# Kernel tuning notes

Measured on AMD Instinct MI355X. Metric: run time of the kernel, lower is better.

## Reference

```python
import jax, jax.numpy as jnp
import numpy as np

B, LAT, ADIM, NACT, H = 131072, 64, 16, 9, 128

def setup_inputs() -> dict:
    key = jax.random.key(0)
    ks = jax.random.split(key, 24)
    p = lambda k, shp: (jax.random.normal(k, shp, dtype=jnp.float32) * 0.05)
    return {
        "z_t": jax.random.normal(ks[0], (B, LAT), dtype=jnp.float32),
        "action": jax.random.randint(ks[1], (B,), 0, NACT),
        "hidden": jnp.zeros((1, B, H), dtype=jnp.float32),
        "embed": p(ks[2], (NACT, ADIM)),
        "fuse_W": p(ks[3], (H, LAT + ADIM)), "fuse_b": p(ks[4], (H,)),
        "W_ih": p(ks[5], (3 * H, H)), "W_hh": p(ks[6], (3 * H, H)),
        "b_ih": p(ks[7], (3 * H,)), "b_hh": p(ks[8], (3 * H,)),
        "ns_W1": p(ks[9], (H, H)), "ns_b1": p(ks[10], (H,)),
        "ns_W2": p(ks[11], (LAT, H)), "ns_b2": p(ks[12], (LAT,)),
        "rw_W1": p(ks[13], (H // 2, H)), "rw_b1": p(ks[14], (H // 2,)),
        "rw_W2": p(ks[15], (1, H // 2)), "rw_b2": p(ks[16], (1,)),
        "dn_W1": p(ks[17], (H // 2, H)), "dn_b1": p(ks[18], (H // 2,)),
        "dn_W2": p(ks[19], (1, H // 2)), "dn_b2": p(ks[20], (1,)),
    }

def _mlp2(x, W1, b1, W2, b2):
    return jax.nn.relu(x @ W1.T + b1) @ W2.T + b2

def reference(z_t, action, hidden, embed, fuse_W, fuse_b, W_ih, W_hh, b_ih, b_hh,
              ns_W1, ns_b1, ns_W2, ns_b2, rw_W1, rw_b1, rw_W2, rw_b2,
              dn_W1, dn_b1, dn_W2, dn_b2):
    a_emb = embed[action]                                  # [B, ADIM]
    fused = jnp.concatenate([z_t, a_emb], axis=-1)         # [B, LAT+ADIM]
    x = jax.nn.relu(fused @ fuse_W.T + fuse_b)             # [B, H]
    h0 = hidden[0]                                         # [B, H]
    gi = x @ W_ih.T + b_ih                                 # [B, 3H]
    gh = h0 @ W_hh.T + b_hh                                # [B, 3H]
    Hd = x.shape[-1]
    r = jax.nn.sigmoid(gi[:, :Hd] + gh[:, :Hd])
    zg = jax.nn.sigmoid(gi[:, Hd:2 * Hd] + gh[:, Hd:2 * Hd])
    n = jnp.tanh(gi[:, 2 * Hd:] + r * gh[:, 2 * Hd:])
    h_new = (1.0 - zg) * n + zg * h0                       # [B, H]
    out = h_new
    z_next = _mlp2(out, ns_W1, ns_b1, ns_W2, ns_b2)        # [B, LAT]
    reward = _mlp2(out, rw_W1, rw_b1, rw_W2, rw_b2)        # [B, 1]
    done_logit = _mlp2(out, dn_W1, dn_b1, dn_W2, dn_b2)    # [B, 1]
    return (z_next, reward, done_logit, h_new[None])
```

## Files before the change

kernel.cpp:

```cpp
#include <hip/hip_runtime.h>
#include <hip/hip_bf16.h>
#include <cstddef>
#include <cstdint>

#define BATCH 131072
#define HOFF ((size_t)BATCH * 66)

typedef __attribute__((ext_vector_type(8))) short short8;
typedef __attribute__((ext_vector_type(4))) short short4v;
typedef __attribute__((ext_vector_type(4))) float f32x4;

typedef const __attribute__((address_space(1))) unsigned int* gas_t;
typedef __attribute__((address_space(3))) unsigned int* las_t;

#define WS_GRU   13312
#define WS_HEAD  119808
#define WS_ELEMS 165888

#define MFMA(a,b,c) __builtin_amdgcn_mfma_f32_16x16x32_bf16((a),(b),(c),0,0,0)

__device__ __forceinline__ short f2bf(float x) {
    __hip_bfloat16 b = __float2bfloat16(x);
    return __builtin_bit_cast(short, b);
}
__device__ __forceinline__ float bf2f(short s) {
    unsigned u = ((unsigned)(unsigned short)s) << 16;
    return __builtin_bit_cast(float, u);
}
__device__ __forceinline__ float fsigmoid(float x) { return __builtin_amdgcn_rcpf(1.0f + __expf(-x)); }
__device__ __forceinline__ float ftanh(float x)    { return 1.0f - 2.0f * __builtin_amdgcn_rcpf(1.0f + __expf(2.0f * x)); }

__device__ __forceinline__ short8 packbf(f32x4 a, f32x4 b) {
    short8 r;
    r[0]=f2bf(a[0]); r[1]=f2bf(a[1]); r[2]=f2bf(a[2]); r[3]=f2bf(a[3]);
    r[4]=f2bf(b[0]); r[5]=f2bf(b[1]); r[6]=f2bf(b[2]); r[7]=f2bf(b[3]);
    return r;
}

template<int NCH>
__device__ __forceinline__ void stage_lds(const short* __restrict__ src, short* dst, int t) {
    constexpr int NP = (NCH + 511) / 512;
    #pragma unroll
    for (int k = 0; k < NP; ++k) {
        int c = t + 512 * k;
        if ((NCH % 512 == 0) || c < NCH)
            __builtin_amdgcn_global_load_lds((gas_t)(const void*)(src + (size_t)c * 8),
                                             (las_t)(void*)(dst + (size_t)c * 8), 16, 0, 0);
    }
}

extern "C" __global__ void prep_weights(const float* __restrict__ fuse_W,
                                        const float* __restrict__ W_ih, const float* __restrict__ W_hh,
                                        const float* __restrict__ ns_W1, const float* __restrict__ ns_W2,
                                        const float* __restrict__ rw_W1, const float* __restrict__ dn_W1,
                                        short* __restrict__ ws) {
    int i = blockIdx.x * 256 + threadIdx.x;
    if (i >= WS_ELEMS) return;
    float v = 0.f;
    if (i < WS_GRU) {
        int j = i / 104, k = i % 104;
        if (k < 80) v = fuse_W[j*80 + k];
    } else if (i < WS_HEAD) {
        int g = (i - WS_GRU) / 6656, e = (i - WS_GRU) % 6656;
        int r = e / 136, k = e % 136;
        if (r < 48 && k < 128) {
            int j = g >> 1;
            const float* W = (g & 1) ? W_hh : W_ih;
            int gate = r >> 4, rr = r & 15;
            v = W[(size_t)(gate*128 + j*16 + rr)*128 + k];
        }
    } else {
        int h = (i - WS_HEAD) / 4608, e = (i - WS_HEAD) % 4608;
        int r = e / 136, k = e % 136;
        if (r < 32 && k < 128) {
            const float* W; int rb;
            if (h < 4)      { W = ns_W1; rb = h*32; }
            else if (h < 6) { W = ns_W2; rb = (h-4)*32; }
            else if (h < 8) { W = rw_W1; rb = (h-6)*32; }
            else            { W = dn_W1; rb = (h-8)*32; }
            v = W[(size_t)(rb + r)*128 + k];
        }
    }
    ws[i] = f2bf(v);
}

#define HEAD_GEMM(FRAG, BIAS, Q, HALFOFF, SP, RELU) do {                                   \
    _Pragma("unroll") for (int sub = 0; sub < 2; ++sub) {                                  \
        float bb = (BIAS)[(Q)*32 + sub*16 + lo];                                           \
        f32x4 a0 = zz4, a1 = zz4;                                                          \
        _Pragma("unroll") for (int kt = 0; kt < 4; ++kt) {                                 \
            short8 Bf = *(const short8*)&smem[(HALFOFF) + (sub*16+lo)*136 + kt*32 + hi*8]; \
            a0 = MFMA((FRAG)[0][kt], Bf, a0); a1 = MFMA((FRAG)[1][kt], Bf, a1); }          \
        _Pragma("unroll") for (int e = 0; e < 4; ++e) {                                    \
            float v0 = a0[e] + bb, v1 = a1[e] + bb;                                        \
            if (RELU) { v0 = fmaxf(v0, 0.f); v1 = fmaxf(v1, 0.f); }                        \
            (SP)[(4*hi+e)*40 + sub*16 + lo]      = f2bf(v0);                               \
            (SP)[(16+4*hi+e)*40 + sub*16 + lo]   = f2bf(v1); }                             \
    } } while (0)

#define AFRAG_READ(DST, Q, SP) do {                                    \
    (DST)[0][Q] = *(const short8*)&(SP)[lo*40 + hi*8];                 \
    (DST)[1][Q] = *(const short8*)&(SP)[(16+lo)*40 + hi*8]; } while (0)

extern "C" __global__ __launch_bounds__(512, 2)
void gru_mfma(const float* __restrict__ z_t, const int* __restrict__ action,
              const float* __restrict__ hidden, const float* __restrict__ embed,
              const float* __restrict__ fuse_b,
              const float* __restrict__ b_ih, const float* __restrict__ b_hh,
              const float* __restrict__ ns_b1, const float* __restrict__ ns_b2,
              const float* __restrict__ rw_b1, const float* __restrict__ rw_W2, const float* __restrict__ rw_b2,
              const float* __restrict__ dn_b1, const float* __restrict__ dn_W2, const float* __restrict__ dn_b2,
              const short* __restrict__ ws, float* out)
{
    __shared__ __align__(16) short smem[33792];

    const int t    = threadIdx.x;
    const int lane = t & 63;
    const int w    = t >> 6;
    const int lo   = lane & 15;
    const int hi   = lane >> 4;
    const int R    = blockIdx.x * 256 + w * 32;
    short* const S0 = &smem[13312 + w * 2560];
    short* const S1 = S0 + 1280;

    const f32x4 zz4 = {0.f, 0.f, 0.f, 0.f};

    auto store_hnew_strip = [&](const short* SP, int kt) {
        #pragma unroll
        for (int v = 0; v < 4; ++v) {
            int idx = v*64 + lane;
            int r = idx >> 3, c = (idx & 7) * 4;
            short4v s = *(const short4v*)&SP[r*40 + c];
            f32x4 f = { bf2f(s[0]), bf2f(s[1]), bf2f(s[2]), bf2f(s[3]) };
            *(f32x4*)&out[HOFF + (size_t)(R + r)*128 + kt*32 + c] = f;
        }
    };
    auto store_z_strip = [&](const short* SP, int q) {
        #pragma unroll
        for (int v = 0; v < 4; ++v) {
            int idx = v*64 + lane;
            int r = idx >> 3, c = (idx & 7) * 4;
            short4v s = *(const short4v*)&SP[r*40 + c];
            f32x4 f = { bf2f(s[0]), bf2f(s[1]), bf2f(s[2]), bf2f(s[3]) };
            *(f32x4*)&out[(size_t)(R + r)*64 + q*32 + c] = f;
        }
    };
    auto head1_dot = [&](const float* W2, float b2) -> float {
        int rr = lane & 31;
        float acc = b2;
        #pragma unroll
        for (int kk = 0; kk < 64; kk += 8) {
            const short* SP = (kk < 32) ? S0 : S1;
            short8 s = *(const short8*)&SP[rr*40 + (kk & 31)];
            f32x4 w0 = *(const f32x4*)&W2[kk];
            f32x4 w1 = *(const f32x4*)&W2[kk+4];
            acc += bf2f(s[0])*w0[0] + bf2f(s[1])*w0[1] + bf2f(s[2])*w0[2] + bf2f(s[3])*w0[3]
                 + bf2f(s[4])*w1[0] + bf2f(s[5])*w1[1] + bf2f(s[6])*w1[2] + bf2f(s[7])*w1[3];
        }
        return acc;
    };

    stage_lds<1664>(ws, &smem[0], t);

    short8 fa[2][3];
    short8 ha[2][4];
    #pragma unroll
    for (int rt = 0; rt < 2; ++rt) {
        const int row = R + rt*16 + lo;
        #pragma unroll
        for (int kt = 0; kt < 2; ++kt) {
            f32x4 p0 = *(const f32x4*)&z_t[(size_t)row*64 + kt*32 + hi*8];
            f32x4 p1 = *(const f32x4*)&z_t[(size_t)row*64 + kt*32 + hi*8 + 4];
            fa[rt][kt] = packbf(p0, p1);
        }
        if (hi < 2) {
            int a = action[row];
            f32x4 e0 = *(const f32x4*)&embed[a*16 + hi*8];
            f32x4 e1 = *(const f32x4*)&embed[a*16 + hi*8 + 4];
            fa[rt][2] = packbf(e0, e1);
        } else {
            short8 z8 = {0,0,0,0,0,0,0,0};
            fa[rt][2] = z8;
        }
        #pragma unroll
        for (int kt = 0; kt < 4; ++kt) {
            f32x4 p0 = *(const f32x4*)&hidden[(size_t)row*128 + kt*32 + hi*8];
            f32x4 p1 = *(const f32x4*)&hidden[(size_t)row*128 + kt*32 + hi*8 + 4];
            ha[rt][kt] = packbf(p0, p1);
        }
    }
    float fbv[8];
    #pragma unroll
    for (int ct = 0; ct < 8; ++ct) fbv[ct] = fuse_b[ct*16 + lo];

    unsigned h0d[8][2][2];
    #pragma unroll
    for (int kt = 0; kt < 4; ++kt) {
        short* SP = (kt & 1) ? S1 : S0;
        *(short8*)&SP[lo*40 + hi*8]        = ha[0][kt];
        *(short8*)&SP[(16 + lo)*40 + hi*8] = ha[1][kt];
        #pragma unroll
        for (int c = 0; c < 2; ++c) {
            int j = 2*kt + c;
            #pragma unroll
            for (int rt = 0; rt < 2; ++rt)
                #pragma unroll
                for (int p = 0; p < 2; ++p) {
                    unsigned a = (unsigned short)SP[(rt*16 + 4*hi + 2*p    )*40 + c*16 + lo];
                    unsigned b = (unsigned short)SP[(rt*16 + 4*hi + 2*p + 1)*40 + c*16 + lo];
                    h0d[j][rt][p] = a | (b << 16);
                }
        }
    }
    __syncthreads();

    short8 xa[2][4];
    #pragma unroll
    for (int kt = 0; kt < 2; ++kt) {
        short* SP = (kt & 1) ? S1 : S0;
        #pragma unroll
        for (int c = 0; c < 2; ++c) {
            int ct = kt*2 + c;
            f32x4 a0 = zz4, a1 = zz4;
            #pragma unroll
            for (int fk = 0; fk < 3; ++fk) {
                short8 B = *(const short8*)&smem[(ct*16 + lo)*104 + fk*32 + hi*8];
                a0 = MFMA(fa[0][fk], B, a0);
                a1 = MFMA(fa[1][fk], B, a1);
            }
            #pragma unroll
            for (int e = 0; e < 4; ++e) {
                SP[(4*hi + e)*40 + c*16 + lo]      = f2bf(fmaxf(a0[e] + fbv[ct], 0.f));
                SP[(16 + 4*hi + e)*40 + c*16 + lo] = f2bf(fmaxf(a1[e] + fbv[ct], 0.f));
            }
        }
        AFRAG_READ(xa, kt, SP);
    }
    __syncthreads();
    stage_lds<832>(ws + WS_GRU, &smem[0], t);

    #pragma unroll
    for (int kt = 2; kt < 4; ++kt) {
        short* SP = (kt & 1) ? S1 : S0;
        #pragma unroll
        for (int c = 0; c < 2; ++c) {
            int ct = kt*2 + c;
            f32x4 a0 = zz4, a1 = zz4;
            #pragma unroll
            for (int fk = 0; fk < 3; ++fk) {
                short8 B = *(const short8*)&smem[6656 + ((ct - 4)*16 + lo)*104 + fk*32 + hi*8];
                a0 = MFMA(fa[0][fk], B, a0);
                a1 = MFMA(fa[1][fk], B, a1);
            }
            #pragma unroll
            for (int e = 0; e < 4; ++e) {
                SP[(4*hi + e)*40 + c*16 + lo]      = f2bf(fmaxf(a0[e] + fbv[ct], 0.f));
                SP[(16 + 4*hi + e)*40 + c*16 + lo] = f2bf(fmaxf(a1[e] + fbv[ct], 0.f));
            }
        }
        AFRAG_READ(xa, kt, SP);
    }
    __syncthreads();

    short8 hfa[2][4];
    #pragma unroll
    for (int j = 0; j < 8; ++j) {
        stage_lds<832>(ws + WS_GRU + (size_t)(2*j + 1)*6656, &smem[6656], t);
        if (j == 2) { AFRAG_READ(hfa, 0, S0); store_hnew_strip(S0, 0); }
        if (j == 4) { AFRAG_READ(hfa, 1, S1); store_hnew_strip(S1, 1); }
        const int j0 = j * 16;
        const float bir = b_ih[j0+lo], biz = b_ih[128+j0+lo], bin = b_ih[256+j0+lo];
        const float bhr = b_hh[j0+lo], bhz = b_hh[128+j0+lo], bhn = b_hh[256+j0+lo];
        f32x4 accI[3][2];
        #pragma unroll
        for (int g = 0; g < 3; ++g) {
            accI[g][0] = zz4; accI[g][1] = zz4;
            #pragma unroll
            for (int kt = 0; kt < 4; ++kt) {
                short8 B = *(const short8*)&smem[(g*16 + lo)*136 + kt*32 + hi*8];
                accI[g][0] = MFMA(xa[0][kt], B, accI[g][0]);
                accI[g][1] = MFMA(xa[1][kt], B, accI[g][1]);
            }
        }
        __syncthreads();

        if (j < 7) stage_lds<832>(ws + WS_GRU + (size_t)(2*j + 2)*6656, &smem[0], t);
        else       stage_lds<576>(ws + WS_HEAD, &smem[0], t);
        f32x4 accH[3][2];
        #pragma unroll
        for (int g = 0; g < 3; ++g) {
            accH[g][0] = zz4; accH[g][1] = zz4;
            #pragma unroll
            for (int kt = 0; kt < 4; ++kt) {
                short8 B = *(const short8*)&smem[6656 + (g*16 + lo)*136 + kt*32 + hi*8];
                accH[g][0] = MFMA(ha[0][kt], B, accH[g][0]);
                accH[g][1] = MFMA(ha[1][kt], B, accH[g][1]);
            }
        }
        {
            short* HP = ((j >> 1) & 1) ? S1 : S0;
            #pragma unroll
            for (int rt = 0; rt < 2; ++rt) {
                #pragma unroll
                for (int p = 0; p < 2; ++p) {
                    unsigned hp = h0d[j][rt][p];
                    float h0a = bf2f((short)(hp & 0xffffu));
                    float h0b = bf2f((short)(hp >> 16));
                    int e = 2*p;
                    {
                        float rg = fsigmoid(accI[0][rt][e] + bir + accH[0][rt][e] + bhr);
                        float zg = fsigmoid(accI[1][rt][e] + biz + accH[1][rt][e] + bhz);
                        float ng = ftanh(accI[2][rt][e] + bin + rg*(accH[2][rt][e] + bhn));
                        HP[(rt*16 + 4*hi + e)*40 + (j&1)*16 + lo] = f2bf((1.f - zg)*ng + zg*h0a);
                    }
                    {
                        float rg = fsigmoid(accI[0][rt][e+1] + bir + accH[0][rt][e+1] + bhr);
                        float zg = fsigmoid(accI[1][rt][e+1] + biz + accH[1][rt][e+1] + bhz);
                        float ng = ftanh(accI[2][rt][e+1] + bin + rg*(accH[2][rt][e+1] + bhn));
                        HP[(rt*16 + 4*hi + e+1)*40 + (j&1)*16 + lo] = f2bf((1.f - zg)*ng + zg*h0b);
                    }
                }
            }
        }
        __syncthreads();
    }

    short8 ta[2][4];

    stage_lds<576>(ws + WS_HEAD + 4608, &smem[6656], t);
    AFRAG_READ(hfa, 2, S0); store_hnew_strip(S0, 2);
    AFRAG_READ(hfa, 3, S1); store_hnew_strip(S1, 3);
    HEAD_GEMM(hfa, ns_b1, 0, 0, S0, true);
    AFRAG_READ(ta, 0, S0);
    __syncthreads();

    stage_lds<576>(ws + WS_HEAD + 2*4608, &smem[0], t);
    HEAD_GEMM(hfa, ns_b1, 1, 6656, S1, true);
    AFRAG_READ(ta, 1, S1);
    __syncthreads();

    stage_lds<576>(ws + WS_HEAD + 3*4608, &smem[6656], t);
    HEAD_GEMM(hfa, ns_b1, 2, 0, S0, true);
    AFRAG_READ(ta, 2, S0);
    __syncthreads();

    stage_lds<576>(ws + WS_HEAD + 4*4608, &smem[0], t);
    HEAD_GEMM(hfa, ns_b1, 3, 6656, S1, true);
    AFRAG_READ(ta, 3, S1);
    __syncthreads();

    stage_lds<576>(ws + WS_HEAD + 5*4608, &smem[6656], t);
    HEAD_GEMM(ta, ns_b2, 0, 0, S0, false);
    store_z_strip(S0, 0);
    __syncthreads();

    stage_lds<576>(ws + WS_HEAD + 6*4608, &smem[0], t);
    HEAD_GEMM(ta, ns_b2, 1, 6656, S1, false);
    store_z_strip(S1, 1);
    __syncthreads();

    stage_lds<576>(ws + WS_HEAD + 7*4608, &smem[6656], t);
    HEAD_GEMM(hfa, rw_b1, 0, 0, S0, true);
    __syncthreads();

    stage_lds<576>(ws + WS_HEAD + 8*4608, &smem[0], t);
    HEAD_GEMM(hfa, rw_b1, 1, 6656, S1, true);
    __syncthreads();

    stage_lds<576>(ws + WS_HEAD + 9*4608, &smem[6656], t);
    {
        float racc = head1_dot(rw_W2, rw_b2[0]);
        if (lane < 32) out[(size_t)BATCH*64 + R + (lane & 31)] = racc;
    }
    HEAD_GEMM(hfa, dn_b1, 0, 0, S0, true);
    __syncthreads();

    HEAD_GEMM(hfa, dn_b1, 1, 6656, S1, true);
    {
        float dacc = head1_dot(dn_W2, dn_b2[0]);
        if (lane < 32) out[(size_t)BATCH*65 + R + (lane & 31)] = dacc;
    }
}

extern "C" void kernel_launch(void* const* d_in, const int* in_sizes, int n_in,
                              void* d_out, int out_size, void* d_ws, size_t ws_size,
                              hipStream_t stream) {
    const float* z_t    = (const float*)d_in[0];
    const int*   action = (const int*)  d_in[1];
    const float* hidden = (const float*)d_in[2];
    const float* embed  = (const float*)d_in[3];
    const float* fuse_W = (const float*)d_in[4];
    const float* fuse_b = (const float*)d_in[5];
    const float* W_ih   = (const float*)d_in[6];
    const float* W_hh   = (const float*)d_in[7];
    const float* b_ih   = (const float*)d_in[8];
    const float* b_hh   = (const float*)d_in[9];
    const float* ns_W1  = (const float*)d_in[10];
    const float* ns_b1  = (const float*)d_in[11];
    const float* ns_W2  = (const float*)d_in[12];
    const float* ns_b2  = (const float*)d_in[13];
    const float* rw_W1  = (const float*)d_in[14];
    const float* rw_b1  = (const float*)d_in[15];
    const float* rw_W2  = (const float*)d_in[16];
    const float* rw_b2  = (const float*)d_in[17];
    const float* dn_W1  = (const float*)d_in[18];
    const float* dn_b1  = (const float*)d_in[19];
    const float* dn_W2  = (const float*)d_in[20];
    const float* dn_b2  = (const float*)d_in[21];
    float* out = (float*)d_out;
    short* ws  = (short*)d_ws;

    hipLaunchKernelGGL(prep_weights, dim3((WS_ELEMS + 255) / 256), dim3(256), 0, stream,
                       fuse_W, W_ih, W_hh, ns_W1, ns_W2, rw_W1, dn_W1, ws);

    hipLaunchKernelGGL(gru_mfma, dim3(BATCH / 256), dim3(512), 0, stream,
                       z_t, action, hidden, embed,
                       fuse_b, b_ih, b_hh, ns_b1, ns_b2,
                       rw_b1, rw_W2, rw_b2, dn_b1, dn_W2, dn_b2,
                       ws, out);
}
```

Measured before the change: 94.16 us.

## Stage GRU and head weights in large LDS chunks to cut block barriers

Enlarges shared memory so half of the GRU weights (8 gate tiles) and, later, all head weights are staged at once, replacing the per-tile double-buffered staging with its many __syncthreads. Each wave now uses a single private strip buffer, and the GRU step is a macro run in two batches of four. Head weight tiles drop their row padding, and the reward/done dot products are computed as partial sums right after each head GEMM. The cost is occupancy: launch bounds go from 2 to 1 block per CU because of the larger LDS footprint, which reduces latency hiding across blocks.

```diff
diff --git a/kernel.cpp b/kernel.cpp
--- a/kernel.cpp
+++ b/kernel.cpp
@@ -14,8 +14,11 @@
 typedef __attribute__((address_space(3))) unsigned int* las_t;
 
 #define WS_GRU   13312
-#define WS_HEAD  119808
-#define WS_ELEMS 165888
+#define WS_HEAD  (13312 + 16*6656)
+#define WS_ELEMS (WS_HEAD + 10*4352)
+
+#define G_BASE   13312
+#define STR_BASE 66560
 
 #define MFMA(a,b,c) __builtin_amdgcn_mfma_f32_16x16x32_bf16((a),(b),(c),0,0,0)
 
@@ -70,9 +73,9 @@
             v = W[(size_t)(gate*128 + j*16 + rr)*128 + k];
         }
     } else {
-        int h = (i - WS_HEAD) / 4608, e = (i - WS_HEAD) % 4608;
+        int h = (i - WS_HEAD) / 4352, e = (i - WS_HEAD) % 4352;
         int r = e / 136, k = e % 136;
-        if (r < 32 && k < 128) {
+        if (k < 128) {
             const float* W; int rb;
             if (h < 4)      { W = ns_W1; rb = h*32; }
             else if (h < 6) { W = ns_W2; rb = (h-4)*32; }
@@ -84,25 +87,60 @@
     ws[i] = f2bf(v);
 }
 
-#define HEAD_GEMM(FRAG, BIAS, Q, HALFOFF, SP, RELU) do {                                   \
-    _Pragma("unroll") for (int sub = 0; sub < 2; ++sub) {                                  \
-        float bb = (BIAS)[(Q)*32 + sub*16 + lo];                                           \
-        f32x4 a0 = zz4, a1 = zz4;                                                          \
-        _Pragma("unroll") for (int kt = 0; kt < 4; ++kt) {                                 \
-            short8 Bf = *(const short8*)&smem[(HALFOFF) + (sub*16+lo)*136 + kt*32 + hi*8]; \
-            a0 = MFMA((FRAG)[0][kt], Bf, a0); a1 = MFMA((FRAG)[1][kt], Bf, a1); }          \
-        _Pragma("unroll") for (int e = 0; e < 4; ++e) {                                    \
-            float v0 = a0[e] + bb, v1 = a1[e] + bb;                                        \
-            if (RELU) { v0 = fmaxf(v0, 0.f); v1 = fmaxf(v1, 0.f); }                        \
-            (SP)[(4*hi+e)*40 + sub*16 + lo]      = f2bf(v0);                               \
-            (SP)[(16+4*hi+e)*40 + sub*16 + lo]   = f2bf(v1); }                             \
+#define HEAD_GEMM(FRAG, BIAS, Q, UBASE, RELU) do {                                          \
+    _Pragma("unroll") for (int sub = 0; sub < 2; ++sub) {                                   \
+        float bb = (BIAS)[(Q)*32 + sub*16 + lo];                                            \
+        f32x4 a0 = zz4, a1 = zz4;                                                           \
+        _Pragma("unroll") for (int kt = 0; kt < 4; ++kt) {                                  \
+            short8 Bf = *(const short8*)&smem[(UBASE) + (sub*16+lo)*136 + kt*32 + hi*8];    \
+            a0 = MFMA((FRAG)[0][kt], Bf, a0); a1 = MFMA((FRAG)[1][kt], Bf, a1); }           \
+        _Pragma("unroll") for (int e = 0; e < 4; ++e) {                                     \
+            float v0 = a0[e] + bb, v1 = a1[e] + bb;                                         \
+            if (RELU) { v0 = fmaxf(v0, 0.f); v1 = fmaxf(v1, 0.f); }                         \
+            S[(4*hi+e)*40 + sub*16 + lo]      = f2bf(v0);                                   \
+            S[(16+4*hi+e)*40 + sub*16 + lo]   = f2bf(v1); }                                 \
     } } while (0)
 
-#define AFRAG_READ(DST, Q, SP) do {                                    \
-    (DST)[0][Q] = *(const short8*)&(SP)[lo*40 + hi*8];                 \
-    (DST)[1][Q] = *(const short8*)&(SP)[(16+lo)*40 + hi*8]; } while (0)
-
-extern "C" __global__ __launch_bounds__(512, 2)
+#define AFRAG_READ(DST, Q) do {                                        \
+    (DST)[0][Q] = *(const short8*)&S[lo*40 + hi*8];                    \
+    (DST)[1][Q] = *(const short8*)&S[(16+lo)*40 + hi*8]; } while (0)
+
+#define GRU_J(JJ) do {                                                                      \
+    const int ihB = G_BASE + (2*((JJ)&3))*6656;                                             \
+    const int hhB = ihB + 6656;                                                             \
+    const int j0 = (JJ)*16;                                                                 \
+    const float bir = b_ih[j0+lo], biz = b_ih[128+j0+lo], bin = b_ih[256+j0+lo];            \
+    const float bhr = b_hh[j0+lo], bhz = b_hh[128+j0+lo], bhn = b_hh[256+j0+lo];            \
+    f32x4 accI[3][2], accH[3][2];                                                           \
+    _Pragma("unroll") for (int g = 0; g < 3; ++g) {                                         \
+        accI[g][0]=zz4; accI[g][1]=zz4; accH[g][0]=zz4; accH[g][1]=zz4;                     \
+        _Pragma("unroll") for (int kt = 0; kt < 4; ++kt) {                                  \
+            short8 Bi = *(const short8*)&smem[ihB + (g*16+lo)*136 + kt*32 + hi*8];          \
+            accI[g][0] = MFMA(xa[0][kt], Bi, accI[g][0]);                                   \
+            accI[g][1] = MFMA(xa[1][kt], Bi, accI[g][1]);                                   \
+            short8 Bh = *(const short8*)&smem[hhB + (g*16+lo)*136 + kt*32 + hi*8];          \
+            accH[g][0] = MFMA(ha[0][kt], Bh, accH[g][0]);                                   \
+            accH[g][1] = MFMA(ha[1][kt], Bh, accH[g][1]);                                   \
+        }                                                                                   \
+    }                                                                                       \
+    _Pragma("unroll") for (int rt = 0; rt < 2; ++rt)                                        \
+    _Pragma("unroll") for (int p = 0; p < 2; ++p) {                                         \
+        unsigned hp = h0d[JJ][rt][p];                                                       \
+        float h0a = bf2f((short)(hp & 0xffffu));                                            \
+        float h0b = bf2f((short)(hp >> 16));                                                \
+        int e = 2*p;                                                                        \
+        { float rg = fsigmoid(accI[0][rt][e] + bir + accH[0][rt][e] + bhr);                 \
+          float zg = fsigmoid(accI[1][rt][e] + biz + accH[1][rt][e] + bhz);                 \
+          float ng = ftanh(accI[2][rt][e] + bin + rg*(accH[2][rt][e] + bhn));               \
+          S[(rt*16 + 4*hi + e)*40 + ((JJ)&1)*16 + lo] = f2bf((1.f-zg)*ng + zg*h0a); }       \
+        { float rg = fsigmoid(accI[0][rt][e+1] + bir + accH[0][rt][e+1] + bhr);             \
+          float zg = fsigmoid(accI[1][rt][e+1] + biz + accH[1][rt][e+1] + bhz);             \
+          float ng = ftanh(accI[2][rt][e+1] + bin + rg*(accH[2][rt][e+1] + bhn));           \
+          S[(rt*16 + 4*hi + e+1)*40 + ((JJ)&1)*16 + lo] = f2bf((1.f-zg)*ng + zg*h0b); }     \
+    }                                                                                       \
+} while (0)
+
+extern "C" __global__ __launch_bounds__(512, 1)
 void gru_mfma(const float* __restrict__ z_t, const int* __restrict__ action,
               const float* __restrict__ hidden, const float* __restrict__ embed,
               const float* __restrict__ fuse_b,
@@ -112,7 +150,7 @@
               const float* __restrict__ dn_b1, const float* __restrict__ dn_W2, const float* __restrict__ dn_b2,
               const short* __restrict__ ws, float* out)
 {
-    __shared__ __align__(16) short smem[33792];
+    __shared__ __align__(16) short smem[76800];
 
     const int t    = threadIdx.x;
     const int lane = t & 63;
@@ -120,38 +158,35 @@
     const int lo   = lane & 15;
     const int hi   = lane >> 4;
     const int R    = blockIdx.x * 256 + w * 32;
-    short* const S0 = &smem[13312 + w * 2560];
-    short* const S1 = S0 + 1280;
+    short* const S = &smem[STR_BASE + w * 1280];
 
     const f32x4 zz4 = {0.f, 0.f, 0.f, 0.f};
 
-    auto store_hnew_strip = [&](const short* SP, int kt) {
+    auto store_hnew_strip = [&](int kt) {
         #pragma unroll
         for (int v = 0; v < 4; ++v) {
             int idx = v*64 + lane;
             int r = idx >> 3, c = (idx & 7) * 4;
-            short4v s = *(const short4v*)&SP[r*40 + c];
+            short4v s = *(const short4v*)&S[r*40 + c];
             f32x4 f = { bf2f(s[0]), bf2f(s[1]), bf2f(s[2]), bf2f(s[3]) };
             *(f32x4*)&out[HOFF + (size_t)(R + r)*128 + kt*32 + c] = f;
         }
     };
-    auto store_z_strip = [&](const short* SP, int q) {
+    auto store_z_strip = [&](int q) {
         #pragma unroll
         for (int v = 0; v < 4; ++v) {
             int idx = v*64 + lane;
             int r = idx >> 3, c = (idx & 7) * 4;
-            short4v s = *(const short4v*)&SP[r*40 + c];
+            short4v s = *(const short4v*)&S[r*40 + c];
             f32x4 f = { bf2f(s[0]), bf2f(s[1]), bf2f(s[2]), bf2f(s[3]) };
             *(f32x4*)&out[(size_t)(R + r)*64 + q*32 + c] = f;
         }
     };
-    auto head1_dot = [&](const float* W2, float b2) -> float {
+    auto hpartial = [&](const float* W2, float acc) -> float {
         int rr = lane & 31;
-        float acc = b2;
-        #pragma unroll
-        for (int kk = 0; kk < 64; kk += 8) {
-            const short* SP = (kk < 32) ? S0 : S1;
-            short8 s = *(const short8*)&SP[rr*40 + (kk & 31)];
+        #pragma unroll
+        for (int kk = 0; kk < 32; kk += 8) {
+            short8 s = *(const short8*)&S[rr*40 + kk];
             f32x4 w0 = *(const f32x4*)&W2[kk];
             f32x4 w1 = *(const f32x4*)&W2[kk+4];
             acc += bf2f(s[0])*w0[0] + bf2f(s[1])*w0[1] + bf2f(s[2])*w0[2] + bf2f(s[3])*w0[3]
@@ -161,6 +196,7 @@
     };
 
     stage_lds<1664>(ws, &smem[0], t);
+    stage_lds<6656>(ws + WS_GRU, &smem[G_BASE], t);
 
     short8 fa[2][3];
     short8 ha[2][4];
@@ -196,9 +232,8 @@
     unsigned h0d[8][2][2];
     #pragma unroll
     for (int kt = 0; kt < 4; ++kt) {
-        short* SP = (kt & 1) ? S1 : S0;
-        *(short8*)&SP[lo*40 + hi*8]        = ha[0][kt];
-        *(short8*)&SP[(16 + lo)*40 + hi*8] = ha[1][kt];
+        *(short8*)&S[lo*40 + hi*8]        = ha[0][kt];
+        *(short8*)&S[(16 + lo)*40 + hi*8] = ha[1][kt];
         #pragma unroll
         for (int c = 0; c < 2; ++c) {
             int j = 2*kt + c;
@@ -206,8 +241,8 @@
             for (int rt = 0; rt < 2; ++rt)
                 #pragma unroll
                 for (int p = 0; p < 2; ++p) {
-                    unsigned a = (unsigned short)SP[(rt*16 + 4*hi + 2*p    )*40 + c*16 + lo];
-                    unsigned b = (unsigned short)SP[(rt*16 + 4*hi + 2*p + 1)*40 + c*16 + lo];
+                    unsigned a = (unsigned short)S[(rt*16 + 4*hi + 2*p    )*40 + c*16 + lo];
+                    unsigned b = (unsigned short)S[(rt*16 + 4*hi + 2*p + 1)*40 + c*16 + lo];
                     h0d[j][rt][p] = a | (b << 16);
                 }
         }
@@ -216,8 +251,7 @@
 
     short8 xa[2][4];
     #pragma unroll
-    for (int kt = 0; kt < 2; ++kt) {
-        short* SP = (kt & 1) ? S1 : S0;
+    for (int kt = 0; kt < 4; ++kt) {
         #pragma unroll
         for (int c = 0; c < 2; ++c) {
             int ct = kt*2 + c;
@@ -230,156 +264,49 @@
             }
             #pragma unroll
             for (int e = 0; e < 4; ++e) {
-                SP[(4*hi + e)*40 + c*16 + lo]      = f2bf(fmaxf(a0[e] + fbv[ct], 0.f));
-                SP[(16 + 4*hi + e)*40 + c*16 + lo] = f2bf(fmaxf(a1[e] + fbv[ct], 0.f));
+                S[(4*hi + e)*40 + c*16 + lo]      = f2bf(fmaxf(a0[e] + fbv[ct], 0.f));
+                S[(16 + 4*hi + e)*40 + c*16 + lo] = f2bf(fmaxf(a1[e] + fbv[ct], 0.f));
             }
         }
-        AFRAG_READ(xa, kt, SP);
-    }
-    __syncthreads();
-    stage_lds<832>(ws + WS_GRU, &smem[0], t);
-
-    #pragma unroll
-    for (int kt = 2; kt < 4; ++kt) {
-        short* SP = (kt & 1) ? S1 : S0;
-        #pragma unroll
-        for (int c = 0; c < 2; ++c) {
-            int ct = kt*2 + c;
-            f32x4 a0 = zz4, a1 = zz4;
-            #pragma unroll
-            for (int fk = 0; fk < 3; ++fk) {
-                short8 B = *(const short8*)&smem[6656 + ((ct - 4)*16 + lo)*104 + fk*32 + hi*8];
-                a0 = MFMA(fa[0][fk], B, a0);
-                a1 = MFMA(fa[1][fk], B, a1);
-            }
-            #pragma unroll
-            for (int e = 0; e < 4; ++e) {
-                SP[(4*hi + e)*40 + c*16 + lo]      = f2bf(fmaxf(a0[e] + fbv[ct], 0.f));
-                SP[(16 + 4*hi + e)*40 + c*16 + lo] = f2bf(fmaxf(a1[e] + fbv[ct], 0.f));
-            }
-        }
-        AFRAG_READ(xa, kt, SP);
-    }
-    __syncthreads();
+        AFRAG_READ(xa, kt);
+    }
 
     short8 hfa[2][4];
-    #pragma unroll
-    for (int j = 0; j < 8; ++j) {
-        stage_lds<832>(ws + WS_GRU + (size_t)(2*j + 1)*6656, &smem[6656], t);
-        if (j == 2) { AFRAG_READ(hfa, 0, S0); store_hnew_strip(S0, 0); }
-        if (j == 4) { AFRAG_READ(hfa, 1, S1); store_hnew_strip(S1, 1); }
-        const int j0 = j * 16;
-        const float bir = b_ih[j0+lo], biz = b_ih[128+j0+lo], bin = b_ih[256+j0+lo];
-        const float bhr = b_hh[j0+lo], bhz = b_hh[128+j0+lo], bhn = b_hh[256+j0+lo];
-        f32x4 accI[3][2];
-        #pragma unroll
-        for (int g = 0; g < 3; ++g) {
-            accI[g][0] = zz4; accI[g][1] = zz4;
-            #pragma unroll
-            for (int kt = 0; kt < 4; ++kt) {
-                short8 B = *(const short8*)&smem[(g*16 + lo)*136 + kt*32 + hi*8];
-                accI[g][0] = MFMA(xa[0][kt], B, accI[g][0]);
-                accI[g][1] = MFMA(xa[1][kt], B, accI[g][1]);
-            }
-        }
-        __syncthreads();
-
-        if (j < 7) stage_lds<832>(ws + WS_GRU + (size_t)(2*j + 2)*6656, &smem[0], t);
-        else       stage_lds<576>(ws + WS_HEAD, &smem[0], t);
-        f32x4 accH[3][2];
-        #pragma unroll
-        for (int g = 0; g < 3; ++g) {
-            accH[g][0] = zz4; accH[g][1] = zz4;
-            #pragma unroll
-            for (int kt = 0; kt < 4; ++kt) {
-                short8 B = *(const short8*)&smem[6656 + (g*16 + lo)*136 + kt*32 + hi*8];
-                accH[g][0] = MFMA(ha[0][kt], B, accH[g][0]);
-                accH[g][1] = MFMA(ha[1][kt], B, accH[g][1]);
-            }
-        }
-        {
-            short* HP = ((j >> 1) & 1) ? S1 : S0;
-            #pragma unroll
-            for (int rt = 0; rt < 2; ++rt) {
-                #pragma unroll
-                for (int p = 0; p < 2; ++p) {
-                    unsigned hp = h0d[j][rt][p];
-                    float h0a = bf2f((short)(hp & 0xffffu));
-                    float h0b = bf2f((short)(hp >> 16));
-                    int e = 2*p;
-                    {
-                        float rg = fsigmoid(accI[0][rt][e] + bir + accH[0][rt][e] + bhr);
-                        float zg = fsigmoid(accI[1][rt][e] + biz + accH[1][rt][e] + bhz);
-                        float ng = ftanh(accI[2][rt][e] + bin + rg*(accH[2][rt][e] + bhn));
-                        HP[(rt*16 + 4*hi + e)*40 + (j&1)*16 + lo] = f2bf((1.f - zg)*ng + zg*h0a);
-                    }
-                    {
-                        float rg = fsigmoid(accI[0][rt][e+1] + bir + accH[0][rt][e+1] + bhr);
-                        float zg = fsigmoid(accI[1][rt][e+1] + biz + accH[1][rt][e+1] + bhz);
-                        float ng = ftanh(accI[2][rt][e+1] + bin + rg*(accH[2][rt][e+1] + bhn));
-                        HP[(rt*16 + 4*hi + e+1)*40 + (j&1)*16 + lo] = f2bf((1.f - zg)*ng + zg*h0b);
-                    }
-                }
-            }
-        }
-        __syncthreads();
-    }
+    GRU_J(0);
+    GRU_J(1); AFRAG_READ(hfa, 0); store_hnew_strip(0);
+    GRU_J(2);
+    GRU_J(3); AFRAG_READ(hfa, 1); store_hnew_strip(1);
+
+    __syncthreads();
+    stage_lds<6656>(ws + WS_GRU + 8*6656, &smem[G_BASE], t);
+    __syncthreads();
+
+    GRU_J(4);
+    GRU_J(5); AFRAG_READ(hfa, 2); store_hnew_strip(2);
+    GRU_J(6);
+    GRU_J(7); AFRAG_READ(hfa, 3); store_hnew_strip(3);
+
+    __syncthreads();
+    stage_lds<5440>(ws + WS_HEAD, &smem[G_BASE], t);
+    __syncthreads();
 
     short8 ta[2][4];
-
-    stage_lds<576>(ws + WS_HEAD + 4608, &smem[6656], t);
-    AFRAG_READ(hfa, 2, S0); store_hnew_strip(S0, 2);
-    AFRAG_READ(hfa, 3, S1); store_hnew_strip(S1, 3);
-    HEAD_GEMM(hfa, ns_b1, 0, 0, S0, true);
-    AFRAG_READ(ta, 0, S0);
-    __syncthreads();
-
-    stage_lds<576>(ws + WS_HEAD + 2*4608, &smem[0], t);
-    HEAD_GEMM(hfa, ns_b1, 1, 6656, S1, true);
-    AFRAG_READ(ta, 1, S1);
-    __syncthreads();
-
-    stage_lds<576>(ws + WS_HEAD + 3*4608, &smem[6656], t);
-    HEAD_GEMM(hfa, ns_b1, 2, 0, S0, true);
-    AFRAG_READ(ta, 2, S0);
-    __syncthreads();
-
-    stage_lds<576>(ws + WS_HEAD + 4*4608, &smem[0], t);
-    HEAD_GEMM(hfa, ns_b1, 3, 6656, S1, true);
-    AFRAG_READ(ta, 3, S1);
-    __syncthreads();
-
-    stage_lds<576>(ws + WS_HEAD + 5*4608, &smem[6656], t);
-    HEAD_GEMM(ta, ns_b2, 0, 0, S0, false);
-    store_z_strip(S0, 0);
-    __syncthreads();
-
-    stage_lds<576>(ws + WS_HEAD + 6*4608, &smem[0], t);
-    HEAD_GEMM(ta, ns_b2, 1, 6656, S1, false);
-    store_z_strip(S1, 1);
-    __syncthreads();
-
-    stage_lds<576>(ws + WS_HEAD + 7*4608, &smem[6656], t);
-    HEAD_GEMM(hfa, rw_b1, 0, 0, S0, true);
-    __syncthreads();
-
-    stage_lds<576>(ws + WS_HEAD + 8*4608, &smem[0], t);
-    HEAD_GEMM(hfa, rw_b1, 1, 6656, S1, true);
-    __syncthreads();
-
-    stage_lds<576>(ws + WS_HEAD + 9*4608, &smem[6656], t);
-    {
-        float racc = head1_dot(rw_W2, rw_b2[0]);
-        if (lane < 32) out[(size_t)BATCH*64 + R + (lane & 31)] = racc;
-    }
-    HEAD_GEMM(hfa, dn_b1, 0, 0, S0, true);
-    __syncthreads();
-
-    HEAD_GEMM(hfa, dn_b1, 1, 6656, S1, true);
-    {
-        float dacc = head1_dot(dn_W2, dn_b2[0]);
-        if (lane < 32) out[(size_t)BATCH*65 + R + (lane & 31)] = dacc;
-    }
+    HEAD_GEMM(hfa, ns_b1, 0, G_BASE + 0*4352, true);  AFRAG_READ(ta, 0);
+    HEAD_GEMM(hfa, ns_b1, 1, G_BASE + 1*4352, true);  AFRAG_READ(ta, 1);
+    HEAD_GEMM(hfa, ns_b1, 2, G_BASE + 2*4352, true);  AFRAG_READ(ta, 2);
+    HEAD_GEMM(hfa, ns_b1, 3, G_BASE + 3*4352, true);  AFRAG_READ(ta, 3);
+    HEAD_GEMM(ta,  ns_b2, 0, G_BASE + 4*4352, false); store_z_strip(0);
+    HEAD_GEMM(ta,  ns_b2, 1, G_BASE + 5*4352, false); store_z_strip(1);
+
+    float racc = rw_b2[0];
+    HEAD_GEMM(hfa, rw_b1, 0, G_BASE + 6*4352, true);  racc = hpartial(rw_W2, racc);
+    HEAD_GEMM(hfa, rw_b1, 1, G_BASE + 7*4352, true);  racc = hpartial(rw_W2 + 32, racc);
+    if (lane < 32) out[(size_t)BATCH*64 + R + (lane & 31)] = racc;
+
+    float dacc = dn_b2[0];
+    HEAD_GEMM(hfa, dn_b1, 0, G_BASE + 8*4352, true);  dacc = hpartial(dn_W2, dacc);
+    HEAD_GEMM(hfa, dn_b1, 1, G_BASE + 9*4352, true);  dacc = hpartial(dn_W2 + 32, dacc);
+    if (lane < 32) out[(size_t)BATCH*65 + R + (lane & 31)] = dacc;
 }
 
 extern "C" void kernel_launch(void* const* d_in, const int* in_sizes, int n_in,
```

Result: faster. 83.72 us (-11.1%).
